# Performance work log

Measured on AMD Instinct MI355X. Metric: run time of the kernel, lower is better.

Reference implementation:

```python
import jax, jax.numpy as jnp
import numpy as np

NUM_GROUPS = 32
EPS = 1e-5
HEAD_DIM = 64

def group_norm(x, w, b):
    # x: [B,C,H,W]; normalize within 32 groups over (C//32, H, W)
    B, C, H, W = x.shape
    xg = x.reshape(B, NUM_GROUPS, C // NUM_GROUPS, H, W)
    mu = xg.mean(axis=(2, 3, 4), keepdims=True)
    var = xg.var(axis=(2, 3, 4), keepdims=True)
    xn = ((xg - mu) / jnp.sqrt(var + EPS)).reshape(B, C, H, W)
    return xn * w[None, :, None, None] + b[None, :, None, None]

def conv1x1(x, w, b):
    # w: [Cout, Cin], b: [Cout]
    return jnp.einsum('bchw,oc->bohw', x, w) + b[None, :, None, None]

def setup_inputs() -> dict:
    key = jax.random.key(0)
    ks = jax.random.split(key, 12)
    B, C, Cc, H, W = 16, 512, 512, 32, 32
    s = 0.02
    return {
        'x': jax.random.normal(ks[0], (B, C, H, W), jnp.float32),
        'context': jax.random.normal(ks[1], (B, Cc, H, W), jnp.float32),
        'norm_q_w': jnp.ones((C,), jnp.float32),
        'norm_q_b': jnp.zeros((C,), jnp.float32),
        'norm_kv_w': jnp.ones((Cc,), jnp.float32),
        'norm_kv_b': jnp.zeros((Cc,), jnp.float32),
        'conv_q_w': jax.random.normal(ks[2], (C, C), jnp.float32) * s,
        'conv_q_b': jnp.zeros((C,), jnp.float32),
        'conv_kv_w': jax.random.normal(ks[3], (2 * C, Cc), jnp.float32) * s,
        'conv_kv_b': jnp.zeros((2 * C,), jnp.float32),
        'proj_w': jax.random.normal(ks[4], (C, C), jnp.float32) * s,
        'proj_b': jnp.zeros((C,), jnp.float32),
    }

def reference(x, context, norm_q_w, norm_q_b, norm_kv_w, norm_kv_b,
              conv_q_w, conv_q_b, conv_kv_w, conv_kv_b, proj_w, proj_b):
    B, C, H, W = x.shape
    nh = max(1, C // HEAD_DIM)
    hd = C // nh
    q = conv1x1(group_norm(x, norm_q_w, norm_q_b), conv_q_w, conv_q_b)
    kv = conv1x1(group_norm(context, norm_kv_w, norm_kv_b), conv_kv_w, conv_kv_b)
    k, v = jnp.split(kv, 2, axis=1)
    L = H * W
    q = q.reshape(B, nh, hd, L)
    k = k.reshape(B, nh, hd, L)
    v = v.reshape(B, nh, hd, L)
    attn = jnp.einsum('bhdi,bhdj->bhij', q, k) * (hd ** -0.5)
    attn = jax.nn.softmax(attn, axis=-1)
    out = jnp.einsum('bhij,bhdj->bhdi', attn, v)
    return x + conv1x1(out.reshape(B, C, H, W), proj_w, proj_b)
```

## Files before the change

### kernel.cpp

```cpp
#include <hip/hip_runtime.h>
#include <hip/hip_bf16.h>

typedef short v8s __attribute__((ext_vector_type(8)));
typedef float v4f __attribute__((ext_vector_type(4)));
typedef float v16f __attribute__((ext_vector_type(16)));
typedef __hip_bfloat16 bf16;

__device__ __forceinline__ float b2f(bf16 h) { return __bfloat162float(h); }
__device__ __forceinline__ bf16 f2b(float f) { return __float2bfloat16(f); }

#define QSCALE 0.18033688f

__device__ __forceinline__ void gll16(const void* g, void* l) {
    __builtin_amdgcn_global_load_lds(
        (const __attribute__((address_space(1))) void*)g,
        (__attribute__((address_space(3))) void*)l, 16, 0, 0);
}

__device__ __forceinline__ unsigned cvtpk(float lo, float hi_) {
    unsigned r;
    asm("v_cvt_pk_bf16_f32 %0, %1, %2" : "=v"(r) : "v"(lo), "v"(hi_));
    return r;
}

__device__ __forceinline__ void pl32swap(unsigned& a, unsigned& b) {
    asm("v_permlane32_swap_b32 %0, %1" : "+v"(a), "+v"(b));
}

__global__ __launch_bounds__(256) void gn_t_kernel(
    const float* __restrict__ x, const float* __restrict__ ctx,
    const float* __restrict__ qw, const float* __restrict__ qb,
    const float* __restrict__ kw, const float* __restrict__ kb,
    bf16* __restrict__ xnT, bf16* __restrict__ cnT)
{
    const int b = blockIdx.y, g = blockIdx.x, z = blockIdx.z, c0 = g * 16;
    const float* src = z ? ctx : x;
    const float* gw  = z ? kw : qw;
    const float* gb  = z ? kb : qb;
    bf16* dst = z ? cnT : xnT;
    __shared__ __attribute__((aligned(16))) bf16 lx[16][1032];
    __shared__ float rS[4], rQ[4];
    __shared__ float sSc[16], sSh[16];
    const int t = threadIdx.x, wave = t >> 6, lane = t & 63;
    const float* xb = src + ((long)b * 512 + c0) * 1024;
    float sum = 0.f, sq = 0.f;
#pragma unroll
    for (int i = 0; i < 16; i++) {
        int q = t + i * 256;
        int ci = q >> 8, l0 = (q & 255) * 4;
        float4 v = *(const float4*)(xb + (long)ci * 1024 + l0);
        sum += v.x + v.y + v.z + v.w;
        sq  += v.x * v.x + v.y * v.y + v.z * v.z + v.w * v.w;
        union { short4 s4v; bf16 h[4]; } w;
        w.h[0] = f2b(v.x); w.h[1] = f2b(v.y); w.h[2] = f2b(v.z); w.h[3] = f2b(v.w);
        *(short4*)&lx[ci][l0] = w.s4v;
    }
#pragma unroll
    for (int off = 32; off > 0; off >>= 1) {
        sum += __shfl_down(sum, off);
        sq  += __shfl_down(sq, off);
    }
    if (lane == 0) { rS[wave] = sum; rQ[wave] = sq; }
    __syncthreads();
    if (t < 16) {
        float S = rS[0] + rS[1] + rS[2] + rS[3];
        float Q = rQ[0] + rQ[1] + rQ[2] + rQ[3];
        const float inv_n = 1.f / 16384.f;
        float mean = S * inv_n;
        float var  = Q * inv_n - mean * mean;
        float rstd = rsqrtf(var + 1e-5f);
        float w = gw[c0 + t];
        sSc[t] = rstd * w;
        sSh[t] = gb[c0 + t] - mean * rstd * w;
    }
    __syncthreads();
#pragma unroll
    for (int i = 0; i < 8; i++) {
        int p = t + i * 256;
        int l = p >> 1, half = (p & 1) * 8;
        union { float4 f4; bf16 h[8]; } o_;
#pragma unroll
        for (int j = 0; j < 8; j++) {
            float y = b2f(lx[half + j][l]) * sSc[half + j] + sSh[half + j];
            o_.h[j] = f2b(y);
        }
        *(float4*)(dst + ((long)b * 1024 + l) * 512 + c0 + half) = o_.f4;
    }
}

__global__ __launch_bounds__(256) void wconv_kernel(
    const float* __restrict__ a, const float* __restrict__ bsrc,
    const float* __restrict__ csrc, bf16* __restrict__ oa,
    bf16* __restrict__ ob, bf16* __restrict__ oc)
{
    int id = blockIdx.x * 256 + threadIdx.x;
    const float* src; bf16* dst; int off;
    if (id < 65536)       { src = a;    dst = oa; off = id; }
    else if (id < 196608) { src = bsrc; dst = ob; off = id - 65536; }
    else                  { src = csrc; dst = oc; off = id - 196608; }
    float4 v = ((const float4*)src)[off];
    union { short4 s4v; bf16 h[4]; } w;
    w.h[0] = f2b(v.x); w.h[1] = f2b(v.y); w.h[2] = f2b(v.z); w.h[3] = f2b(v.w);
    ((short4*)dst)[off] = w.s4v;
}

__global__ __launch_bounds__(256) void qkv_gemm_kernel(
    const bf16* __restrict__ xnT, const bf16* __restrict__ cnT,
    const bf16* __restrict__ wQ, const bf16* __restrict__ wKV,
    bf16* __restrict__ QT, bf16* __restrict__ KT, bf16* __restrict__ Vo,
    const float* __restrict__ cqb, const float* __restrict__ ckvb)
{
    const long PB = 512L * 1024;
    const int blk = blockIdx.x;
    const int xcd = blk & 7, idx = blk >> 3;
    const int half = idx / 96, rr = idx % 96;
    const int op = rr >> 5, bx = rr & 31;
    const int bz = xcd + 8 * half;
    const bf16* A; const bf16* B; bf16* C; const float* bias;
    int nBlkN, N, biasPerM; float scale;
    if (op == 0) {
        A = xnT + bz * PB; B = wQ;  C = QT + bz * PB; bias = cqb;
        nBlkN = 4; N = 512; biasPerM = 0; scale = QSCALE;
    } else if (op == 1) {
        A = cnT + bz * PB; B = wKV; C = KT + bz * PB; bias = ckvb;
        nBlkN = 4; N = 512; biasPerM = 0; scale = 1.0f;
    } else {
        A = wKV + 512L * 512; B = cnT + bz * PB; C = Vo + bz * PB; bias = ckvb + 512;
        nBlkN = 8; N = 1024; biasPerM = 1; scale = 1.0f;
    }
    const int m0 = (bx / nBlkN) * 128, n0 = (bx % nBlkN) * 128;
    __shared__ __attribute__((aligned(16))) bf16 lA[2][128][64];
    __shared__ __attribute__((aligned(16))) bf16 lB[2][128][64];
    const int t = threadIdx.x, wave = t >> 6, lane = t & 63;
    const int quad = lane >> 4, c = lane & 15;
    const int wm = (wave >> 1) * 64, wn = (wave & 1) * 64;
    const int rIS = lane >> 3;
    const int chG = (lane & 7) ^ rIS;
    const bf16* Ag[4]; const bf16* Bg[4]; int segr[4];
#pragma unroll
    for (int j = 0; j < 4; j++) {
        int seg = wave + j * 4;
        segr[j] = seg * 8;
        Ag[j] = A + (long)(m0 + segr[j] + rIS) * 512 + chG * 8;
        Bg[j] = B + (long)(n0 + segr[j] + rIS) * 512 + chG * 8;
    }
    auto issue = [&](int k0, int bi) {
#pragma unroll
        for (int j = 0; j < 4; j++) {
            gll16(Ag[j] + k0, &lA[bi][segr[j]][0]);
            gll16(Bg[j] + k0, &lB[bi][segr[j]][0]);
        }
    };
    v4f acc[4][4] = {};
    issue(0, 0);
    for (int kc = 0; kc < 8; kc++) {
        const int cur = kc & 1;
        asm volatile("s_waitcnt vmcnt(0)" ::: "memory");
        __builtin_amdgcn_s_barrier();
        __builtin_amdgcn_sched_barrier(0);
        if (kc < 7) issue((kc + 1) * 64, cur ^ 1);
#pragma unroll
        for (int kk = 0; kk < 2; kk++) {
            v8s af[4], bfr[4];
#pragma unroll
            for (int mt = 0; mt < 4; mt++)
                af[mt] = *(const v8s*)&lA[cur][wm + mt * 16 + c][((kk * 4 + quad) ^ (c & 7)) * 8];
#pragma unroll
            for (int nt = 0; nt < 4; nt++)
                bfr[nt] = *(const v8s*)&lB[cur][wn + nt * 16 + c][((kk * 4 + quad) ^ (c & 7)) * 8];
#pragma unroll
            for (int mt = 0; mt < 4; mt++)
#pragma unroll
                for (int nt = 0; nt < 4; nt++)
                    acc[mt][nt] = __builtin_amdgcn_mfma_f32_16x16x32_bf16(
                        af[mt], bfr[nt], acc[mt][nt], 0, 0, 0);
        }
    }
#pragma unroll
    for (int mt = 0; mt < 4; mt++) {
#pragma unroll
        for (int nt = 0; nt < 4; nt++) {
#pragma unroll
            for (int r = 0; r < 4; r++) {
                int row = m0 + wm + mt * 16 + quad * 4 + r;
                int col = n0 + wn + nt * 16 + c;
                float v = (acc[mt][nt][r] + (biasPerM ? bias[row] : bias[col])) * scale;
                C[(long)row * N + col] = f2b(v);
            }
        }
    }
}

__global__ __launch_bounds__(256) void gemm_proj_kernel(
    const bf16* __restrict__ A,
    const bf16* __restrict__ B, long sBb,
    float* __restrict__ C,
    const float* __restrict__ bias,
    const float* __restrict__ resid,
    int M, int N)
{
    const int bz = blockIdx.z;
    const int m0 = blockIdx.x * 128, n0 = blockIdx.y * 128;
    const bf16* Bb = B + (long)bz * sBb;
    __shared__ __attribute__((aligned(16))) bf16 lA[128][64];
    __shared__ __attribute__((aligned(16))) bf16 lB[128][64];
    const int t = threadIdx.x, wave = t >> 6, lane = t & 63;
    const int quad = lane >> 4, c = lane & 15;
    const int wm = (wave >> 1) * 64, wn = (wave & 1) * 64;
    const int rIS = lane >> 3, chG = (lane & 7) ^ rIS;
    const bf16* Ag[4]; const bf16* Bg[4];
    bf16* Al[4]; bf16* Bl[4];
#pragma unroll
    for (int j = 0; j < 4; j++) {
        int seg = wave + j * 4;
        int row = seg * 8 + rIS;
        Ag[j] = A + (long)(m0 + row) * 512 + chG * 8;
        Bg[j] = Bb + (long)(n0 + row) * 512 + chG * 8;
        Al[j] = &lA[seg * 8][0];
        Bl[j] = &lB[seg * 8][0];
    }
    v4f acc[4][4] = {};
    for (int k0 = 0; k0 < 512; k0 += 64) {
        __syncthreads();
#pragma unroll
        for (int j = 0; j < 4; j++) {
            gll16(Ag[j] + k0, Al[j]);
            gll16(Bg[j] + k0, Bl[j]);
        }
        __syncthreads();
#pragma unroll
        for (int kk = 0; kk < 2; kk++) {
            v8s af[4], bfr[4];
#pragma unroll
            for (int mt = 0; mt < 4; mt++)
                af[mt] = *(const v8s*)&lA[wm + mt * 16 + c][((kk * 4 + quad) ^ (c & 7)) * 8];
#pragma unroll
            for (int nt = 0; nt < 4; nt++)
                bfr[nt] = *(const v8s*)&lB[wn + nt * 16 + c][((kk * 4 + quad) ^ (c & 7)) * 8];
#pragma unroll
            for (int mt = 0; mt < 4; mt++)
#pragma unroll
                for (int nt = 0; nt < 4; nt++)
                    acc[mt][nt] = __builtin_amdgcn_mfma_f32_16x16x32_bf16(
                        af[mt], bfr[nt], acc[mt][nt], 0, 0, 0);
        }
    }
#pragma unroll
    for (int mt = 0; mt < 4; mt++) {
#pragma unroll
        for (int nt = 0; nt < 4; nt++) {
#pragma unroll
            for (int r = 0; r < 4; r++) {
                int row = m0 + wm + mt * 16 + quad * 4 + r;
                int col = n0 + wn + nt * 16 + c;
                float v = acc[mt][nt][r] + bias[row]
                        + resid[(long)bz * ((long)M * N) + (long)row * N + col];
                C[(long)bz * ((long)M * N) + (long)row * N + col] = v;
            }
        }
    }
}

__global__ __launch_bounds__(256, 2) void attn_kernel(
    const bf16* QT, const bf16* __restrict__ KT,
    const bf16* __restrict__ V, bf16* AOT)
{
    const int nblk = blockIdx.x;
    const int s = nblk >> 3;
    const int it = s & 3;
    const int g = ((s >> 2) << 3) | (nblk & 7);
    const int h = g & 7, b = g >> 3;
    const int i0 = it * 256;
    __shared__ __attribute__((aligned(16))) bf16 lk[3][64][64];
    __shared__ __attribute__((aligned(16))) bf16 lv[3][64][64];
    const int t = threadIdx.x, wave = t >> 6, lane = t & 63;
    const int m31 = lane & 31, hi = lane >> 5;
    const int rIS = lane >> 3, chG = (lane & 7) ^ rIS;
    v8s qf[2][4];
#pragma unroll
    for (int iq = 0; iq < 2; iq++) {
        const bf16* Qb = QT + ((long)b * 1024 + i0 + wave * 64 + iq * 32 + m31) * 512 + h * 64;
#pragma unroll
        for (int ks = 0; ks < 4; ks++)
            qf[iq][ks] = *(const v8s*)(Qb + ks * 16 + hi * 8);
    }
    const bf16* Kg[2]; const bf16* Vg[2];
#pragma unroll
    for (int j = 0; j < 2; j++) {
        int seg = wave * 2 + j;
        Kg[j] = KT + ((long)b * 1024 + seg * 8 + rIS) * 512 + h * 64 + chG * 8;
        Vg[j] = V + ((long)b * 512 + h * 64 + seg * 8 + rIS) * 1024 + chG * 8;
    }
    auto issue = [&](int jtx, int bi) {
#pragma unroll
        for (int j = 0; j < 2; j++) {
            int seg = wave * 2 + j;
            gll16(Kg[j] + (long)jtx * 64 * 512, &lk[bi][seg * 8][0]);
            gll16(Vg[j] + (long)jtx * 64,      &lv[bi][seg * 8][0]);
        }
    };
    issue(0, 0);
    issue(1, 1);
    float lsum0 = 0.f, lsum1 = 0.f;
    v16f o00 = {}, o01 = {}, o10 = {}, o11 = {};

#define SMPV(sj0, sj1, JB)                                                     \
    {                                                                          \
        unsigned u0[8], u1[8];                                                 \
        _Pragma("unroll")                                                      \
        for (int k2 = 0; k2 < 8; k2++) {                                       \
            float p0l = __builtin_amdgcn_exp2f(sj0[2 * k2]);                   \
            float p0h = __builtin_amdgcn_exp2f(sj0[2 * k2 + 1]);               \
            float p1l = __builtin_amdgcn_exp2f(sj1[2 * k2]);                   \
            float p1h = __builtin_amdgcn_exp2f(sj1[2 * k2 + 1]);               \
            lsum0 += p0l + p0h; lsum1 += p1l + p1h;                            \
            u0[k2] = cvtpk(p0l, p0h); u1[k2] = cvtpk(p1l, p1h);                \
        }                                                                      \
        pl32swap(u0[0], u0[2]); pl32swap(u0[1], u0[3]);                        \
        pl32swap(u0[4], u0[6]); pl32swap(u0[5], u0[7]);                        \
        pl32swap(u1[0], u1[2]); pl32swap(u1[1], u1[3]);                        \
        pl32swap(u1[4], u1[6]); pl32swap(u1[5], u1[7]);                        \
        __builtin_amdgcn_s_setprio(1);                                         \
        _Pragma("unroll")                                                      \
        for (int kk = 0; kk < 2; kk++) {                                       \
            union { unsigned w[4]; v8s v; } pf0, pf1;                          \
            pf0.w[0] = u0[4 * kk + 0]; pf0.w[1] = u0[4 * kk + 1];              \
            pf0.w[2] = u0[4 * kk + 2]; pf0.w[3] = u0[4 * kk + 3];              \
            pf1.w[0] = u1[4 * kk + 0]; pf1.w[1] = u1[4 * kk + 1];              \
            pf1.w[2] = u1[4 * kk + 2]; pf1.w[3] = u1[4 * kk + 3];              \
            const int cc2 = ((JB) * 2 + kk) * 2 + hi;                          \
            v8s vf0 = *(const v8s*)&lv[cur][m31][(cc2 ^ (m31 & 7)) * 8];       \
            o00 = __builtin_amdgcn_mfma_f32_32x32x16_bf16(vf0, pf0.v, o00, 0, 0, 0); \
            o10 = __builtin_amdgcn_mfma_f32_32x32x16_bf16(vf0, pf1.v, o10, 0, 0, 0); \
            v8s vf1 = *(const v8s*)&lv[cur][32 + m31][(cc2 ^ (m31 & 7)) * 8];  \
            o01 = __builtin_amdgcn_mfma_f32_32x32x16_bf16(vf1, pf0.v, o01, 0, 0, 0); \
            o11 = __builtin_amdgcn_mfma_f32_32x32x16_bf16(vf1, pf1.v, o11, 0, 0, 0); \
        }                                                                      \
        __builtin_amdgcn_s_setprio(0);                                         \
    }

    for (int jt = 0; jt < 16; jt++) {
        const int cur = jt % 3;
        asm volatile("s_waitcnt vmcnt(4)" ::: "memory");
        __builtin_amdgcn_s_barrier();
        __builtin_amdgcn_sched_barrier(0);
        issue((jt + 2) & 15, (jt + 2) % 3);
        v16f s00 = {}, s01 = {}, s10 = {}, s11 = {};
        __builtin_amdgcn_s_setprio(1);
#pragma unroll
        for (int ks = 0; ks < 4; ks++) {
            const int chs = ((ks * 2 + hi) ^ (m31 & 7)) * 8;
            v8s kf0 = *(const v8s*)&lk[cur][m31][chs];
            v8s kf1 = *(const v8s*)&lk[cur][32 + m31][chs];
            s00 = __builtin_amdgcn_mfma_f32_32x32x16_bf16(kf0, qf[0][ks], s00, 0, 0, 0);
            s01 = __builtin_amdgcn_mfma_f32_32x32x16_bf16(kf0, qf[1][ks], s01, 0, 0, 0);
            s10 = __builtin_amdgcn_mfma_f32_32x32x16_bf16(kf1, qf[0][ks], s10, 0, 0, 0);
            s11 = __builtin_amdgcn_mfma_f32_32x32x16_bf16(kf1, qf[1][ks], s11, 0, 0, 0);
        }
        __builtin_amdgcn_s_setprio(0);
        SMPV(s00, s01, 0)
        SMPV(s10, s11, 1)
    }
#undef SMPV
    {
        float lt0 = lsum0 + __shfl_xor(lsum0, 32);
        float lt1 = lsum1 + __shfl_xor(lsum1, 32);
        float inv0 = 1.f / lt0, inv1 = 1.f / lt1;
#pragma unroll
        for (int iq = 0; iq < 2; iq++) {
            float inv = iq ? inv1 : inv0;
            const v16f& oa = iq ? o10 : o00;
            const v16f& ob = iq ? o11 : o01;
            bf16* Ob = AOT + ((long)b * 1024 + i0 + wave * 64 + iq * 32 + m31) * 512 + h * 64;
#pragma unroll
            for (int gq = 0; gq < 4; gq++) {
                union { short4 s4v; bf16 hh[4]; } w0, w1;
#pragma unroll
                for (int k = 0; k < 4; k++) {
                    w0.hh[k] = f2b(oa[gq * 4 + k] * inv);
                    w1.hh[k] = f2b(ob[gq * 4 + k] * inv);
                }
                *(short4*)(Ob + gq * 8 + hi * 4)      = w0.s4v;
                *(short4*)(Ob + 32 + gq * 8 + hi * 4) = w1.s4v;
            }
        }
    }
}

extern "C" void kernel_launch(void* const* d_in, const int* in_sizes, int n_in,
                              void* d_out, int out_size, void* d_ws, size_t ws_size,
                              hipStream_t stream)
{
    const float* x    = (const float*)d_in[0];
    const float* ctx  = (const float*)d_in[1];
    const float* nqw  = (const float*)d_in[2];
    const float* nqb  = (const float*)d_in[3];
    const float* nkw  = (const float*)d_in[4];
    const float* nkb  = (const float*)d_in[5];
    const float* cqw  = (const float*)d_in[6];
    const float* cqb  = (const float*)d_in[7];
    const float* ckvw = (const float*)d_in[8];
    const float* ckvb = (const float*)d_in[9];
    const float* pw   = (const float*)d_in[10];
    const float* pb   = (const float*)d_in[11];
    float* out = (float*)d_out;
    bf16* ws  = (bf16*)d_ws;

    const long PB  = 512L * 1024;
    const long TOT = 16L * PB;
    bf16* s0 = ws;
    bf16* s1 = ws + TOT;
    bf16* s2 = ws + 2 * TOT;
    bf16* s3 = ws + 3 * TOT;
    bf16* s4 = ws + 4 * TOT;
    bf16* wQ  = ws + 5 * TOT;
    bf16* wKV = wQ + 262144;
    bf16* wP  = wKV + 524288;

    dim3 blk(256);
    gn_t_kernel<<<dim3(32, 16, 2), blk, 0, stream>>>(
        x, ctx, nqw, nqb, nkw, nkb, s0, s1);
    wconv_kernel<<<dim3(1024), blk, 0, stream>>>(cqw, ckvw, pw, wQ, wKV, wP);
    qkv_gemm_kernel<<<dim3(1536), blk, 0, stream>>>(
        s0, s1, wQ, wKV, s2, s3, s4, cqb, ckvb);
    attn_kernel<<<dim3(512), blk, 0, stream>>>(s2, s3, s4, s2);
    gemm_proj_kernel<<<dim3(4, 8, 16), blk, 0, stream>>>(
        wP, s2, PB, out, pb, x, 512, 1024);
}
```

Measured before the change: 240.1 us.

## Double-buffer proj GEMM LDS loads, remap grid for XCD locality, vectorize GN store

The projection GEMM now keeps two LDS buffers and issues the next K-chunk's global-to-LDS loads before computing on the current one, so memory latency overlaps with the MFMA work. It launches as a flat 1D grid whose block index is decoded so that each XCD handles its own batch slices, which should improve L2 locality. The group-norm transpose store now reads 8 channel rows as vector LDS loads and writes 8 positions per thread, cutting scalar LDS reads. The double buffer doubles LDS use to 64KB per block, which may reduce occupancy.

```diff
diff --git a/kernel.cpp b/kernel.cpp
--- a/kernel.cpp
+++ b/kernel.cpp
@@ -74,17 +74,26 @@
         sSh[t] = gb[c0 + t] - mean * rstd * w;
     }
     __syncthreads();
-#pragma unroll
-    for (int i = 0; i < 8; i++) {
-        int p = t + i * 256;
-        int l = p >> 1, half = (p & 1) * 8;
-        union { float4 f4; bf16 h[8]; } o_;
+    {
+        const int hf = t & 1, lg = t >> 1;
+        const int ch0 = hf * 8, l0 = lg * 8;
+        v8s rd[8];
+#pragma unroll
+        for (int r = 0; r < 8; r++)
+            rd[r] = *(const v8s*)&lx[ch0 + r][l0];
+        float sc[8], sh[8];
+#pragma unroll
+        for (int r = 0; r < 8; r++) { sc[r] = sSc[ch0 + r]; sh[r] = sSh[ch0 + r]; }
 #pragma unroll
         for (int j = 0; j < 8; j++) {
-            float y = b2f(lx[half + j][l]) * sSc[half + j] + sSh[half + j];
-            o_.h[j] = f2b(y);
-        }
-        *(float4*)(dst + ((long)b * 1024 + l) * 512 + c0 + half) = o_.f4;
+            union { float4 f4; bf16 h[8]; } o_;
+#pragma unroll
+            for (int r = 0; r < 8; r++) {
+                union { short s; bf16 h; } cv; cv.s = rd[r][j];
+                o_.h[r] = f2b(b2f(cv.h) * sc[r] + sh[r]);
+            }
+            *(float4*)(dst + ((long)b * 1024 + l0 + j) * 512 + c0 + ch0) = o_.f4;
+        }
     }
 }
 
@@ -199,44 +208,50 @@
     const float* __restrict__ resid,
     int M, int N)
 {
-    const int bz = blockIdx.z;
-    const int m0 = blockIdx.x * 128, n0 = blockIdx.y * 128;
+    const int blk = blockIdx.x;
+    const int xcd = blk & 7, idx = blk >> 3;
+    const int bz = xcd + 8 * (idx & 1);
+    const int tile = idx >> 1;
+    const int m0 = (tile >> 3) * 128, n0 = (tile & 7) * 128;
     const bf16* Bb = B + (long)bz * sBb;
-    __shared__ __attribute__((aligned(16))) bf16 lA[128][64];
-    __shared__ __attribute__((aligned(16))) bf16 lB[128][64];
+    __shared__ __attribute__((aligned(16))) bf16 lA[2][128][64];
+    __shared__ __attribute__((aligned(16))) bf16 lB[2][128][64];
     const int t = threadIdx.x, wave = t >> 6, lane = t & 63;
     const int quad = lane >> 4, c = lane & 15;
     const int wm = (wave >> 1) * 64, wn = (wave & 1) * 64;
     const int rIS = lane >> 3, chG = (lane & 7) ^ rIS;
-    const bf16* Ag[4]; const bf16* Bg[4];
-    bf16* Al[4]; bf16* Bl[4];
+    const bf16* Ag[4]; const bf16* Bg[4]; int segr[4];
 #pragma unroll
     for (int j = 0; j < 4; j++) {
         int seg = wave + j * 4;
-        int row = seg * 8 + rIS;
-        Ag[j] = A + (long)(m0 + row) * 512 + chG * 8;
-        Bg[j] = Bb + (long)(n0 + row) * 512 + chG * 8;
-        Al[j] = &lA[seg * 8][0];
-        Bl[j] = &lB[seg * 8][0];
-    }
+        segr[j] = seg * 8;
+        Ag[j] = A + (long)(m0 + segr[j] + rIS) * 512 + chG * 8;
+        Bg[j] = Bb + (long)(n0 + segr[j] + rIS) * 512 + chG * 8;
+    }
+    auto issue = [&](int k0, int bi) {
+#pragma unroll
+        for (int j = 0; j < 4; j++) {
+            gll16(Ag[j] + k0, &lA[bi][segr[j]][0]);
+            gll16(Bg[j] + k0, &lB[bi][segr[j]][0]);
+        }
+    };
     v4f acc[4][4] = {};
-    for (int k0 = 0; k0 < 512; k0 += 64) {
-        __syncthreads();
-#pragma unroll
-        for (int j = 0; j < 4; j++) {
-            gll16(Ag[j] + k0, Al[j]);
-            gll16(Bg[j] + k0, Bl[j]);
-        }
-        __syncthreads();
+    issue(0, 0);
+    for (int kc = 0; kc < 8; kc++) {
+        const int cur = kc & 1;
+        asm volatile("s_waitcnt vmcnt(0)" ::: "memory");
+        __builtin_amdgcn_s_barrier();
+        __builtin_amdgcn_sched_barrier(0);
+        if (kc < 7) issue((kc + 1) * 64, cur ^ 1);
 #pragma unroll
         for (int kk = 0; kk < 2; kk++) {
             v8s af[4], bfr[4];
 #pragma unroll
             for (int mt = 0; mt < 4; mt++)
-                af[mt] = *(const v8s*)&lA[wm + mt * 16 + c][((kk * 4 + quad) ^ (c & 7)) * 8];
+                af[mt] = *(const v8s*)&lA[cur][wm + mt * 16 + c][((kk * 4 + quad) ^ (c & 7)) * 8];
 #pragma unroll
             for (int nt = 0; nt < 4; nt++)
-                bfr[nt] = *(const v8s*)&lB[wn + nt * 16 + c][((kk * 4 + quad) ^ (c & 7)) * 8];
+                bfr[nt] = *(const v8s*)&lB[cur][wn + nt * 16 + c][((kk * 4 + quad) ^ (c & 7)) * 8];
 #pragma unroll
             for (int mt = 0; mt < 4; mt++)
 #pragma unroll
@@ -424,6 +439,6 @@
     qkv_gemm_kernel<<<dim3(1536), blk, 0, stream>>>(
         s0, s1, wQ, wKV, s2, s3, s4, cqb, ckvb);
     attn_kernel<<<dim3(512), blk, 0, stream>>>(s2, s3, s4, s2);
-    gemm_proj_kernel<<<dim3(4, 8, 16), blk, 0, stream>>>(
+    gemm_proj_kernel<<<dim3(512), blk, 0, stream>>>(
         wP, s2, PB, out, pb, x, 512, 1024);
 }
```

Result: faster. 234.3 us (-2.4%).
